# Optimization experiments

Hardware: AMD Instinct MI355X
Metric: run time of the kernel (lower is better)

## Reference

```python
import jax, jax.numpy as jnp
import numpy as np

B, N = 1024, 4096
EPS = 1e-4


def setup_inputs() -> dict:
    key = jax.random.key(0)
    k1, k2, k3 = jax.random.split(key, 3)
    src_coords = jax.random.normal(k1, (B, N, 2), dtype=jnp.float32)
    tgt_coords = jax.random.normal(k2, (B, N, 2), dtype=jnp.float32)
    weights = jax.random.uniform(k3, (B, 1, N), dtype=jnp.float32)
    return {"src_coords": src_coords, "tgt_coords": tgt_coords, "weights": weights}


def reference(src_coords, tgt_coords, weights):
    # pad 2D -> 3D (z = 0), matching F.pad(..., [0, pad, 0, 0])
    src = jnp.pad(src_coords, ((0, 0), (0, 0), (0, 1)))  # [B, N, 3]
    tgt = jnp.pad(tgt_coords, ((0, 0), (0, 0), (0, 1)))
    src = src.transpose(0, 2, 1)  # [B, 3, N]
    tgt = tgt.transpose(0, 2, 1)

    w = jnp.sum(weights, axis=2, keepdims=True) + EPS          # [B, 1, 1]
    src_centroid = jnp.sum(src * weights, axis=2, keepdims=True) / w  # [B, 3, 1]
    tgt_centroid = jnp.sum(tgt * weights, axis=2, keepdims=True) / w
    src_centered = src - src_centroid
    tgt_centered = tgt - tgt_centroid

    # weighted cross-covariance: [B, 3, 3]
    W = jnp.einsum('bin,bjn->bij', tgt_centered * weights, src_centered) / w

    U, _, Vh = jnp.linalg.svd(W)  # torch.svd returns V; V^T == Vh
    det_UV = jnp.linalg.det(U) * jnp.linalg.det(Vh)  # det(V) == det(Vh)
    ones = jnp.ones((W.shape[0],), dtype=W.dtype)
    s_diag = jnp.stack([ones, ones, det_UV], axis=1)  # [B, 3]
    # R = U @ diag(s) @ Vh
    R_tgt_src = jnp.einsum('bij,bj,bjk->bik', U, s_diag, Vh)

    t_tgt_src_insrc = src_centroid - jnp.einsum('bji,bjk->bik', R_tgt_src, tgt_centroid)
    t_src_tgt_intgt = -jnp.einsum('bij,bjk->bik', R_tgt_src, t_tgt_src_insrc)
    return (R_tgt_src, t_src_tgt_intgt)
```

## Files before the change

kernel.cpp:

```cpp
#include <hip/hip_runtime.h>


constexpr int BATCH = 1024;
constexpr int NPTS  = 4096;
constexpr int TPB   = 512;
constexpr int PASSES = NPTS / (TPB * 4);
constexpr double EPSV = 1e-4;

__global__ __launch_bounds__(TPB) void procrustes_kernel(
    const float* __restrict__ src, const float* __restrict__ tgt,
    const float* __restrict__ wts, float* __restrict__ out)
{
    const int b   = blockIdx.x;
    const int tid = threadIdx.x;
    const float* sb = src + (size_t)b * (NPTS * 2);
    const float* tb = tgt + (size_t)b * (NPTS * 2);
    const float* wb = wts + (size_t)b * NPTS;

    float4 wv[PASSES], s0[PASSES], s1[PASSES], t0[PASSES], t1[PASSES];
    #pragma unroll
    for (int pass = 0; pass < PASSES; ++pass) {
        const int i = tid * 4 + pass * (TPB * 4);
        wv[pass] = *reinterpret_cast<const float4*>(wb + i);
        s0[pass] = *reinterpret_cast<const float4*>(sb + 2 * i);
        s1[pass] = *reinterpret_cast<const float4*>(sb + 2 * i + 4);
        t0[pass] = *reinterpret_cast<const float4*>(tb + 2 * i);
        t1[pass] = *reinterpret_cast<const float4*>(tb + 2 * i + 4);
    }

    float accf[9] = {0,0,0,0,0,0,0,0,0};

    #pragma unroll
    for (int pass = 0; pass < PASSES; ++pass) {
        const float wf[4]  = {wv[pass].x, wv[pass].y, wv[pass].z, wv[pass].w};
        const float sxf[4] = {s0[pass].x, s0[pass].z, s1[pass].x, s1[pass].z};
        const float syf[4] = {s0[pass].y, s0[pass].w, s1[pass].y, s1[pass].w};
        const float txf[4] = {t0[pass].x, t0[pass].z, t1[pass].x, t1[pass].z};
        const float tyf[4] = {t0[pass].y, t0[pass].w, t1[pass].y, t1[pass].w};

        #pragma unroll
        for (int j = 0; j < 4; ++j) {
            const float w  = wf[j];
            const float sx = sxf[j], sy = syf[j];
            const float tx = txf[j], ty = tyf[j];
            accf[0] += w;
            accf[1] = fmaf(w, sx, accf[1]);
            accf[2] = fmaf(w, sy, accf[2]);
            accf[3] = fmaf(w, tx, accf[3]);
            accf[4] = fmaf(w, ty, accf[4]);
            const float wt0 = w * tx, wt1 = w * ty;
            accf[5] = fmaf(wt0, sx, accf[5]);
            accf[6] = fmaf(wt0, sy, accf[6]);
            accf[7] = fmaf(wt1, sx, accf[7]);
            accf[8] = fmaf(wt1, sy, accf[8]);
        }
    }

    __shared__ float  part[TPB][9];
    __shared__ double p2[9][32];
    __shared__ double sfin[9];

    #pragma unroll
    for (int k = 0; k < 9; ++k) part[tid][k] = accf[k];
    __syncthreads();

    if (tid < 288) {
        const int k = tid >> 5, c = tid & 31;
        double v = 0.0;
        #pragma unroll
        for (int i = 0; i < 16; ++i) v += (double)part[c + 32 * i][k];
        p2[k][c] = v;
    }
    __syncthreads();

    if (tid < 9) {
        double v = 0.0;
        #pragma unroll
        for (int c = 0; c < 32; ++c) v += p2[tid][c];
        sfin[tid] = v;
    }
    __syncthreads();

    if (tid == 0) {
        double s[9];
        #pragma unroll
        for (int k = 0; k < 9; ++k) s[k] = sfin[k];

        const double w   = s[0] + EPSV;
        const double inv = 1.0 / w;
        const double scx = s[1] * inv, scy = s[2] * inv;
        const double tcx = s[3] * inv, tcy = s[4] * inv;

        const double a00 = s[5] - s[3] * s[1] * inv;
        const double a01 = s[6] - s[3] * s[2] * inv;
        const double a10 = s[7] - s[4] * s[1] * inv;
        const double a11 = s[8] - s[4] * s[2] * inv;

        const double p = 0.5 * (a00 + a11);
        const double q = 0.5 * (a10 - a01);
        const double r = 0.5 * (a00 - a11);
        const double t = 0.5 * (a01 + a10);

        const double rot2 = p * p + q * q;
        const double ref2 = r * r + t * t;

        double R00, R01, R10, R11, Rzz;
        if (rot2 >= ref2) {
            const double n = rsqrt(fmax(rot2, 1e-300));
            R00 =  p * n; R01 = -q * n;
            R10 =  q * n; R11 =  p * n;
            Rzz = 1.0;
        } else {
            const double n = rsqrt(fmax(ref2, 1e-300));
            R00 =  r * n; R01 =  t * n;
            R10 =  t * n; R11 = -r * n;
            Rzz = -1.0;
        }

        const double t1x = scx - (R00 * tcx + R10 * tcy);
        const double t1y = scy - (R01 * tcx + R11 * tcy);
        const double t2x = -(R00 * t1x + R01 * t1y);
        const double t2y = -(R10 * t1x + R11 * t1y);

        float* Ro = out + (size_t)b * 9;
        Ro[0] = (float)R00; Ro[1] = (float)R01; Ro[2] = 0.0f;
        Ro[3] = (float)R10; Ro[4] = (float)R11; Ro[5] = 0.0f;
        Ro[6] = 0.0f;       Ro[7] = 0.0f;       Ro[8] = (float)Rzz;

        float* To = out + (size_t)BATCH * 9 + (size_t)b * 3;
        To[0] = (float)t2x; To[1] = (float)t2y; To[2] = 0.0f;
    }
}

extern "C" void kernel_launch(void* const* d_in, const int* in_sizes, int n_in,
                              void* d_out, int out_size, void* d_ws, size_t ws_size,
                              hipStream_t stream) {
    const float* src = (const float*)d_in[0];
    const float* tgt = (const float*)d_in[1];
    const float* wts = (const float*)d_in[2];
    float* out = (float*)d_out;
    procrustes_kernel<<<BATCH, TPB, 0, stream>>>(src, tgt, wts, out);
}
```

Measured before the change: 100.6 us.

## Use packed float2 accumulation and DPP wave reductions instead of LDS tree

The per-thread accumulation now uses two-wide float vectors so the compiler can emit packed FMA instructions. The block reduction replaces the 512x9 shared-memory stage and its 288-thread double-precision pass with DPP row-shift wave sums, followed by a tiny per-wave shared array. This cuts LDS traffic and one barrier. The cost is that partial sums stay in float32 across a whole wave before the double-precision combine, which may slightly change accuracy.

```diff
diff --git a/kernel.cpp b/kernel.cpp
--- a/kernel.cpp
+++ b/kernel.cpp
@@ -6,6 +6,22 @@
 constexpr int TPB   = 512;
 constexpr int PASSES = NPTS / (TPB * 4);
 constexpr double EPSV = 1e-4;
+
+typedef float v2f __attribute__((ext_vector_type(2)));
+
+#define DPP_STEP(x, ctrl)                                                     \
+    (x) += __uint_as_float(__builtin_amdgcn_update_dpp(                        \
+        0, (int)__float_as_uint(x), (ctrl), 0xf, 0xf, true))
+
+__device__ __forceinline__ float wave_sum_dpp(float x) {
+    DPP_STEP(x, 0x111);
+    DPP_STEP(x, 0x112);
+    DPP_STEP(x, 0x114);
+    DPP_STEP(x, 0x118);
+    DPP_STEP(x, 0x142);
+    DPP_STEP(x, 0x143);
+    return x;
+}
 
 __global__ __launch_bounds__(TPB) void procrustes_kernel(
     const float* __restrict__ src, const float* __restrict__ tgt,
@@ -28,55 +44,51 @@
         t1[pass] = *reinterpret_cast<const float4*>(tb + 2 * i + 4);
     }
 
-    float accf[9] = {0,0,0,0,0,0,0,0,0};
+    v2f accS = {0.f, 0.f}, accT = {0.f, 0.f}, accX = {0.f, 0.f}, accY = {0.f, 0.f};
+    float accW = 0.f;
 
     #pragma unroll
     for (int pass = 0; pass < PASSES; ++pass) {
-        const float wf[4]  = {wv[pass].x, wv[pass].y, wv[pass].z, wv[pass].w};
-        const float sxf[4] = {s0[pass].x, s0[pass].z, s1[pass].x, s1[pass].z};
-        const float syf[4] = {s0[pass].y, s0[pass].w, s1[pass].y, s1[pass].w};
-        const float txf[4] = {t0[pass].x, t0[pass].z, t1[pass].x, t1[pass].z};
-        const float tyf[4] = {t0[pass].y, t0[pass].w, t1[pass].y, t1[pass].w};
+        const float wk[4] = {wv[pass].x, wv[pass].y, wv[pass].z, wv[pass].w};
+        const v2f sp[4] = {{s0[pass].x, s0[pass].y}, {s0[pass].z, s0[pass].w},
+                           {s1[pass].x, s1[pass].y}, {s1[pass].z, s1[pass].w}};
+        const v2f tp[4] = {{t0[pass].x, t0[pass].y}, {t0[pass].z, t0[pass].w},
+                           {t1[pass].x, t1[pass].y}, {t1[pass].z, t1[pass].w}};
 
         #pragma unroll
         for (int j = 0; j < 4; ++j) {
-            const float w  = wf[j];
-            const float sx = sxf[j], sy = syf[j];
-            const float tx = txf[j], ty = tyf[j];
-            accf[0] += w;
-            accf[1] = fmaf(w, sx, accf[1]);
-            accf[2] = fmaf(w, sy, accf[2]);
-            accf[3] = fmaf(w, tx, accf[3]);
-            accf[4] = fmaf(w, ty, accf[4]);
-            const float wt0 = w * tx, wt1 = w * ty;
-            accf[5] = fmaf(wt0, sx, accf[5]);
-            accf[6] = fmaf(wt0, sy, accf[6]);
-            accf[7] = fmaf(wt1, sx, accf[7]);
-            accf[8] = fmaf(wt1, sy, accf[8]);
+            const float w = wk[j];
+            const v2f w2  = {w, w};
+            const v2f wt  = w2 * tp[j];
+            accW += w;
+            accT += wt;
+            accS = __builtin_elementwise_fma(w2, sp[j], accS);
+            const v2f wtx = {wt.x, wt.x};
+            accX = __builtin_elementwise_fma(wtx, sp[j], accX);
+            const v2f wty = {wt.y, wt.y};
+            accY = __builtin_elementwise_fma(wty, sp[j], accY);
         }
     }
 
-    __shared__ float  part[TPB][9];
-    __shared__ double p2[9][32];
-    __shared__ double sfin[9];
+    float accf[9] = {accW, accS.x, accS.y, accT.x, accT.y,
+                     accX.x, accX.y, accY.x, accY.y};
 
     #pragma unroll
-    for (int k = 0; k < 9; ++k) part[tid][k] = accf[k];
-    __syncthreads();
+    for (int k = 0; k < 9; ++k) accf[k] = wave_sum_dpp(accf[k]);
 
-    if (tid < 288) {
-        const int k = tid >> 5, c = tid & 31;
-        double v = 0.0;
+    __shared__ float  red[TPB / 64][9];
+    __shared__ double sfin[9];
+    const int lane = tid & 63, wave = tid >> 6;
+    if (lane == 63) {
         #pragma unroll
-        for (int i = 0; i < 16; ++i) v += (double)part[c + 32 * i][k];
-        p2[k][c] = v;
+        for (int k = 0; k < 9; ++k) red[wave][k] = accf[k];
     }
     __syncthreads();
 
     if (tid < 9) {
         double v = 0.0;
         #pragma unroll
-        for (int c = 0; c < 32; ++c) v += p2[tid][c];
+        for (int wv2 = 0; wv2 < TPB / 64; ++wv2) v += (double)red[wv2][tid];
         sfin[tid] = v;
     }
     __syncthreads();
```

After: 100.2 us. No clear change (-0.4%).
